# Kernel optimization log

Measured on AMD Instinct MI355X. Metric: run time of the kernel, lower is better.

The kernel has to match this reference:

```python
import jax, jax.numpy as jnp
import numpy as np

FP8_MAX = 448.0   # torch.finfo(float8_e4m3fn).max
BLK = 128         # block_size = [128, 128] for weights; [1, 128] for activations
E, H, I, T, TOPK = 8, 2048, 1408, 512, 2
FP8 = jnp.float8_e4m3fn


def fp8_round(x):
    """Round-trip through float8_e4m3fn (simulates .to(float8_e4m3fn))."""
    return jnp.clip(x, -FP8_MAX, FP8_MAX).astype(FP8).astype(jnp.float32)


def setup_inputs() -> dict:
    key = jax.random.key(0)
    ks = jax.random.split(key, 7)
    hidden_states = jax.random.normal(ks[0], (T, H), jnp.float32)
    top_k_index = jax.random.randint(ks[1], (T, TOPK), 0, E)
    top_k_weights = jax.random.uniform(ks[2], (T, TOPK), jnp.float32)
    # FP8 weight codes (stored as fp32 values exactly representable in e4m3fn)
    gate_up_proj = fp8_round(jax.random.normal(ks[3], (E, 2 * I, H), jnp.float32))
    gate_up_proj_scale_inv = jax.random.uniform(ks[4], (E, (2 * I) // BLK, H // BLK), jnp.float32, 1e-4, 1e-2)
    down_proj = fp8_round(jax.random.normal(ks[5], (E, H, I), jnp.float32))
    down_proj_scale_inv = jax.random.uniform(ks[6], (E, H // BLK, I // BLK), jnp.float32, 1e-4, 1e-2)
    return {
        "hidden_states": hidden_states,
        "top_k_index": top_k_index,
        "top_k_weights": top_k_weights,
        "gate_up_proj": gate_up_proj,
        "gate_up_proj_scale_inv": gate_up_proj_scale_inv,
        "down_proj": down_proj,
        "down_proj_scale_inv": down_proj_scale_inv,
    }


def dequant_weight(wq, s):
    # wq: [E, N, K] fp8 codes; s: [E, N//BLK, K//BLK] per-128x128-block scale_inv
    e, n, k = wq.shape
    wb = wq.reshape(e, n // BLK, BLK, k // BLK, BLK)
    return (wb * s[:, :, None, :, None]).reshape(e, n, k)


def quant_dequant_act(x):
    # dynamic per-(row, 128-block) fp8 activation quantization, then dequant
    shp = x.shape
    xb = x.reshape(shp[:-1] + (shp[-1] // BLK, BLK))
    amax = jnp.max(jnp.abs(xb), axis=-1, keepdims=True)
    scale = jnp.maximum(amax, 1e-12) / FP8_MAX
    q = fp8_round(xb / scale)
    return (q * scale).reshape(shp)


def reference(hidden_states, top_k_index, top_k_weights, gate_up_proj,
              gate_up_proj_scale_inv, down_proj, down_proj_scale_inv):
    w_gu = dequant_weight(gate_up_proj, gate_up_proj_scale_inv)  # [E, 2I, H]
    w_d = dequant_weight(down_proj, down_proj_scale_inv)         # [E, H, I]
    # activation quantization is per-token-block, so unrouted tokens are
    # unaffected; dense per-expert compute + combine-weight mask equals the
    # original gather/scatter loop exactly (unrouted contributions weight 0).
    x = quant_dequant_act(hidden_states)                         # [T, H]
    gate_up = jnp.einsum('th,enh->etn', x, w_gu)                 # [E, T, 2I]
    gate, up = jnp.split(gate_up, 2, axis=-1)
    h = jax.nn.silu(gate) * up                                   # [E, T, I]
    h = quant_dequant_act(h)
    down = jnp.einsum('eti,ehi->eth', h, w_d)                    # [E, T, H]
    # combine[t, e] = sum over top-k slots routing token t to expert e
    combine = jnp.sum(jax.nn.one_hot(top_k_index, E, dtype=top_k_weights.dtype)
                      * top_k_weights[..., None], axis=1)        # [T, E]
    out = jnp.einsum('eth,te->th', down, combine)
    return out.astype(hidden_states.dtype)
```

## Files before the change

### kernel.cpp

```cpp
#include <hip/hip_runtime.h>
#include <math.h>

#define NE 8
#define HD 2048
#define ID 1408
#define NT 512
#define FP8MAX 448.0f

typedef __attribute__((ext_vector_type(4))) float floatx4;

__device__ __forceinline__ floatx4 fzero4() {
    floatx4 z; z.x = 0.f; z.y = 0.f; z.z = 0.f; z.w = 0.f; return z;
}

#define OFF_OFFS  0
#define OFF_TOK   1024
#define OFF_WGT   8192
#define OFF_ENT   16384
#define OFF_XSG   32768
#define OFF_XG    131072
#define OFF_HS    (3*1024*1024)
#define OFF_HQ    (3*1024*1024 + 65536)
#define OFF_GU0   (5*1024*1024)
#define OFF_GU1   (17*1024*1024)

#define LDA 136

__global__ void route_kernel(const int* __restrict__ tki,
                             const float* __restrict__ tkw,
                             int* __restrict__ offs,
                             int* __restrict__ tok,
                             float* __restrict__ wgt,
                             int* __restrict__ ent) {
    __shared__ int cnt[NE];
    __shared__ int cur[NE];
    __shared__ int base[NE + 1];
    int tid = threadIdx.x;
    if (tid < NE) { cnt[tid] = 0; cur[tid] = 0; }
    __syncthreads();
    int e = tki[tid];
    atomicAdd(&cnt[e], 1);
    __syncthreads();
    if (tid == 0) {
        int s = 0;
        for (int i = 0; i < NE; i++) { base[i] = s; s += cnt[i]; }
        base[NE] = s;
    }
    __syncthreads();
    int pos = atomicAdd(&cur[e], 1);
    int j = base[e] + pos;
    tok[j] = tid >> 1;
    wgt[j] = tkw[tid];
    ent[tid] = j;
    if (tid <= NE) offs[tid] = base[tid];
}

__global__ void quant_x_kernel(const float* __restrict__ x,
                               const int* __restrict__ ent,
                               unsigned char* __restrict__ xg,
                               float* __restrict__ xsg) {
    int wid = (blockIdx.x * 256 + threadIdx.x) >> 6;
    int lane = threadIdx.x & 63;
    int t = wid >> 4;
    int b = wid & 15;
    const float2 v = *(const float2*)(x + (long)t * HD + b * 128 + lane * 2);
    float am = fmaxf(fabsf(v.x), fabsf(v.y));
    #pragma unroll
    for (int m = 32; m; m >>= 1) am = fmaxf(am, __shfl_xor(am, m));
    float scale = fmaxf(am, 1e-12f) / FP8MAX;
    int p = __builtin_amdgcn_cvt_pk_fp8_f32(v.x / scale, v.y / scale, 0, false);
    unsigned short pk = (unsigned short)(p & 0xffff);
    int e0 = ent[2 * t], e1 = ent[2 * t + 1];
    *(unsigned short*)(xg + (long)e0 * HD + b * 128 + lane * 2) = pk;
    *(unsigned short*)(xg + (long)e1 * HD + b * 128 + lane * 2) = pk;
    if (lane == 0) { xsg[e0 * 16 + b] = scale; xsg[e1 * 16 + b] = scale; }
}

__global__ void quant_h_kernel(const float* __restrict__ gu0,
                               const float* __restrict__ gu1,
                               unsigned char* __restrict__ hq,
                               float* __restrict__ hs) {
    int wid = (blockIdx.x * 256 + threadIdx.x) >> 6;
    int lane = threadIdx.x & 63;
    int j = wid / 11;
    int b = wid - j * 11;
    long base = (long)j * 2816 + b * 128 + lane * 2;
    float2 ga = *(const float2*)(gu0 + base);
    float2 gb = *(const float2*)(gu1 + base);
    float2 ua = *(const float2*)(gu0 + base + 1408);
    float2 ub = *(const float2*)(gu1 + base + 1408);
    float gx = ga.x + gb.x, gy = ga.y + gb.y;
    float ux = ua.x + ub.x, uy = ua.y + ub.y;
    float hx = (gx / (1.0f + expf(-gx))) * ux;
    float hy = (gy / (1.0f + expf(-gy))) * uy;
    float am = fmaxf(fabsf(hx), fabsf(hy));
    #pragma unroll
    for (int m = 32; m; m >>= 1) am = fmaxf(am, __shfl_xor(am, m));
    float scale = fmaxf(am, 1e-12f) / FP8MAX;
    int p = __builtin_amdgcn_cvt_pk_fp8_f32(hx / scale, hy / scale, 0, false);
    *(unsigned short*)(hq + (long)j * ID + b * 128 + lane * 2) =
        (unsigned short)(p & 0xffff);
    if (lane == 0) hs[j * 11 + b] = scale;
}

__global__ __launch_bounds__(256, 3) void gemm1_kernel(
    const unsigned char* __restrict__ xg,
    const float* __restrict__ xsg,
    const float* __restrict__ wgu,
    const float* __restrict__ sgu,
    const int* __restrict__ offs,
    float* __restrict__ gu0,
    float* __restrict__ gu1) {
    int e = blockIdx.z;
    int mt = blockIdx.y;
    int jb = blockIdx.x >> 1;
    int kh = blockIdx.x & 1;
    int o0 = offs[e], o1 = offs[e + 1];
    int ne = o1 - o0;
    int m0 = mt * 128;
    if (m0 >= ne) return;
    int rem = ne - m0;
    int j0 = o0 + m0;

    __shared__ __align__(16) unsigned char Asm[128 * LDA];
    __shared__ __align__(16) unsigned char Bsm[64 * LDA];
    __shared__ __align__(16) float sxa[128 * 20];

    int tid = threadIdx.x;
    {
        int r = tid >> 1, q = tid & 1;
        int j = j0 + r; if (j >= o1) j = o0;
        float4 s0 = *(const float4*)(xsg + j * 16 + q * 8);
        float4 s1 = *(const float4*)(xsg + j * 16 + q * 8 + 4);
        *(float4*)&sxa[r * 20 + q * 8] = s0;
        *(float4*)&sxa[r * 20 + q * 8 + 4] = s1;
    }

    int wave = tid >> 6;
    int lane = tid & 63;
    int lr = lane & 15;
    int lq = lane >> 4;

    int aseg = tid & 7;
    int arow0 = tid >> 3;
    const unsigned char* aBase0;
    const unsigned char* aBase1;
    const unsigned char* aBase2;
    const unsigned char* aBase3;
    {
        int j;
        j = j0 + arow0;       if (j >= o1) j = o0; aBase0 = xg + (long)j * HD + aseg * 16;
        j = j0 + 32 + arow0;  if (j >= o1) j = o0; aBase1 = xg + (long)j * HD + aseg * 16;
        j = j0 + 64 + arow0;  if (j >= o1) j = o0; aBase2 = xg + (long)j * HD + aseg * 16;
        j = j0 + 96 + arow0;  if (j >= o1) j = o0; aBase3 = xg + (long)j * HD + aseg * 16;
    }

    int bcol = tid & 31;
    int brow0 = tid >> 5;
    const float* bG = wgu + ((long)e * 2816 + jb * 32 + brow0) * HD + bcol * 4;
    const float* bU = wgu + ((long)e * 2816 + 1408 + jb * 32 + brow0) * HD + bcol * 4;
    const float* sgp = sgu + (e * 22 + (jb >> 2)) * 16;
    const float* sup = sgu + (e * 22 + 11 + (jb >> 2)) * 16;

    floatx4 facc[8];
    #pragma unroll
    for (int i = 0; i < 8; i++) facc[i] = fzero4();

    int kbS = kh * 8, kbE = kbS + 8;

    uint4 a0 = *(const uint4*)(aBase0 + kbS * 128);
    uint4 a1 = *(const uint4*)(aBase1 + kbS * 128);
    uint4 a2 = *(const uint4*)(aBase2 + kbS * 128);
    uint4 a3 = *(const uint4*)(aBase3 + kbS * 128);
    float4 f0 = *(const float4*)(bG + kbS * 128);
    float4 f1 = *(const float4*)(bG + kbS * 128 + 8 * HD);
    float4 f2 = *(const float4*)(bG + kbS * 128 + 16 * HD);
    float4 f3 = *(const float4*)(bG + kbS * 128 + 24 * HD);
    float4 f4 = *(const float4*)(bU + kbS * 128);
    float4 f5 = *(const float4*)(bU + kbS * 128 + 8 * HD);
    float4 f6 = *(const float4*)(bU + kbS * 128 + 16 * HD);
    float4 f7 = *(const float4*)(bU + kbS * 128 + 24 * HD);

    for (int kb = kbS; kb < kbE; kb++) {
        {
            *(uint4*)(&Asm[(arow0)      * LDA + aseg * 16]) = a0;
            *(uint4*)(&Asm[(arow0 + 32) * LDA + aseg * 16]) = a1;
            *(uint4*)(&Asm[(arow0 + 64) * LDA + aseg * 16]) = a2;
            *(uint4*)(&Asm[(arow0 + 96) * LDA + aseg * 16]) = a3;
            int p0 = __builtin_amdgcn_cvt_pk_fp8_f32(f0.x, f0.y, 0, false);
            p0 = __builtin_amdgcn_cvt_pk_fp8_f32(f0.z, f0.w, p0, true);
            int p1 = __builtin_amdgcn_cvt_pk_fp8_f32(f1.x, f1.y, 0, false);
            p1 = __builtin_amdgcn_cvt_pk_fp8_f32(f1.z, f1.w, p1, true);
            int p2 = __builtin_amdgcn_cvt_pk_fp8_f32(f2.x, f2.y, 0, false);
            p2 = __builtin_amdgcn_cvt_pk_fp8_f32(f2.z, f2.w, p2, true);
            int p3 = __builtin_amdgcn_cvt_pk_fp8_f32(f3.x, f3.y, 0, false);
            p3 = __builtin_amdgcn_cvt_pk_fp8_f32(f3.z, f3.w, p3, true);
            int p4 = __builtin_amdgcn_cvt_pk_fp8_f32(f4.x, f4.y, 0, false);
            p4 = __builtin_amdgcn_cvt_pk_fp8_f32(f4.z, f4.w, p4, true);
            int p5 = __builtin_amdgcn_cvt_pk_fp8_f32(f5.x, f5.y, 0, false);
            p5 = __builtin_amdgcn_cvt_pk_fp8_f32(f5.z, f5.w, p5, true);
            int p6 = __builtin_amdgcn_cvt_pk_fp8_f32(f6.x, f6.y, 0, false);
            p6 = __builtin_amdgcn_cvt_pk_fp8_f32(f6.z, f6.w, p6, true);
            int p7 = __builtin_amdgcn_cvt_pk_fp8_f32(f7.x, f7.y, 0, false);
            p7 = __builtin_amdgcn_cvt_pk_fp8_f32(f7.z, f7.w, p7, true);
            *(unsigned int*)(&Bsm[(brow0)      * LDA + bcol * 4]) = (unsigned int)p0;
            *(unsigned int*)(&Bsm[(brow0 + 8)  * LDA + bcol * 4]) = (unsigned int)p1;
            *(unsigned int*)(&Bsm[(brow0 + 16) * LDA + bcol * 4]) = (unsigned int)p2;
            *(unsigned int*)(&Bsm[(brow0 + 24) * LDA + bcol * 4]) = (unsigned int)p3;
            *(unsigned int*)(&Bsm[(brow0 + 32) * LDA + bcol * 4]) = (unsigned int)p4;
            *(unsigned int*)(&Bsm[(brow0 + 40) * LDA + bcol * 4]) = (unsigned int)p5;
            *(unsigned int*)(&Bsm[(brow0 + 48) * LDA + bcol * 4]) = (unsigned int)p6;
            *(unsigned int*)(&Bsm[(brow0 + 56) * LDA + bcol * 4]) = (unsigned int)p7;
        }
        __syncthreads();
        {
            int kn = (kb + 1 < kbE) ? (kb + 1) : kb;
            a0 = *(const uint4*)(aBase0 + kn * 128);
            a1 = *(const uint4*)(aBase1 + kn * 128);
            a2 = *(const uint4*)(aBase2 + kn * 128);
            a3 = *(const uint4*)(aBase3 + kn * 128);
            f0 = *(const float4*)(bG + kn * 128);
            f1 = *(const float4*)(bG + kn * 128 + 8 * HD);
            f2 = *(const float4*)(bG + kn * 128 + 16 * HD);
            f3 = *(const float4*)(bG + kn * 128 + 24 * HD);
            f4 = *(const float4*)(bU + kn * 128);
            f5 = *(const float4*)(bU + kn * 128 + 8 * HD);
            f6 = *(const float4*)(bU + kn * 128 + 16 * HD);
            f7 = *(const float4*)(bU + kn * 128 + 24 * HD);
        }
        floatx4 cacc[8];
        #pragma unroll
        for (int i = 0; i < 8; i++) cacc[i] = fzero4();
        #pragma unroll
        for (int ks = 0; ks < 4; ks++) {
            long a[2], b[4];
            #pragma unroll
            for (int mi = 0; mi < 2; mi++)
                a[mi] = *(const long*)(&Asm[(wave * 32 + mi * 16 + lr) * LDA + ks * 32 + lq * 8]);
            #pragma unroll
            for (int ni = 0; ni < 4; ni++)
                b[ni] = *(const long*)(&Bsm[(ni * 16 + lr) * LDA + ks * 32 + lq * 8]);
            #pragma unroll
            for (int mi = 0; mi < 2; mi++)
                #pragma unroll
                for (int ni = 0; ni < 4; ni++)
                    cacc[mi * 4 + ni] = __builtin_amdgcn_mfma_f32_16x16x32_fp8_fp8(
                        a[mi], b[ni], cacc[mi * 4 + ni], 0, 0, 0);
        }
        float sg = sgp[kb];
        float su = sup[kb];
        #pragma unroll
        for (int mi = 0; mi < 2; mi++) {
            #pragma unroll
            for (int reg = 0; reg < 4; reg++) {
                float sx = sxa[(wave * 32 + mi * 16 + lq * 4 + reg) * 20 + kb];
                #pragma unroll
                for (int ni = 0; ni < 4; ni++) {
                    float sw = (ni < 2) ? sg : su;
                    facc[mi * 4 + ni][reg] += cacc[mi * 4 + ni][reg] * (sw * sx);
                }
            }
        }
        __syncthreads();
    }

    float* gu = kh ? gu1 : gu0;
    #pragma unroll
    for (int mi = 0; mi < 2; mi++) {
        #pragma unroll
        for (int ni = 0; ni < 4; ni++) {
            #pragma unroll
            for (int reg = 0; reg < 4; reg++) {
                int r = wave * 32 + mi * 16 + lq * 4 + reg;
                if (r < rem) {
                    long base = (long)(j0 + r) * 2816;
                    long col = (ni < 2) ? (jb * 32 + ni * 16 + lr)
                                        : (1408 + jb * 32 + (ni - 2) * 16 + lr);
                    gu[base + col] = facc[mi * 4 + ni][reg];
                }
            }
        }
    }
}

__global__ __launch_bounds__(256, 4) void gemm2_kernel(
    const unsigned char* __restrict__ hq,
    const float* __restrict__ hs,
    const float* __restrict__ wd,
    const float* __restrict__ sd,
    const int* __restrict__ offs,
    const int* __restrict__ tok,
    const float* __restrict__ wgt,
    float* __restrict__ out) {
    int e = blockIdx.z;
    int mt = blockIdx.y;
    int jb = blockIdx.x >> 1;
    int kh = blockIdx.x & 1;
    int o0 = offs[e], o1 = offs[e + 1];
    int ne = o1 - o0;
    int m0 = mt * 128;
    if (m0 >= ne) return;
    int rem = ne - m0;
    int j0 = o0 + m0;

    __shared__ __align__(16) unsigned char Asm[128 * LDA];
    __shared__ __align__(16) unsigned char Bsm[32 * LDA];
    __shared__ __align__(16) float sha[128 * 12];
    __shared__ int tokL[128];
    __shared__ float wgtL[128];

    int tid = threadIdx.x;
    if (tid < 128) {
        int j = j0 + tid;
        int valid = j < o1;
        if (!valid) j = o0;
        tokL[tid] = tok[j];
        wgtL[tid] = valid ? wgt[j] : 0.0f;
        const float* s = hs + j * 11;
        #pragma unroll
        for (int k = 0; k < 11; k++) sha[tid * 12 + k] = s[k];
    }

    int wave = tid >> 6;
    int lane = tid & 63;
    int lr = lane & 15;
    int lq = lane >> 4;

    int aseg = tid & 7;
    int arow0 = tid >> 3;
    const unsigned char* aBase0;
    const unsigned char* aBase1;
    const unsigned char* aBase2;
    const unsigned char* aBase3;
    {
        int j;
        j = j0 + arow0;       if (j >= o1) j = o0; aBase0 = hq + (long)j * ID + aseg * 16;
        j = j0 + 32 + arow0;  if (j >= o1) j = o0; aBase1 = hq + (long)j * ID + aseg * 16;
        j = j0 + 64 + arow0;  if (j >= o1) j = o0; aBase2 = hq + (long)j * ID + aseg * 16;
        j = j0 + 96 + arow0;  if (j >= o1) j = o0; aBase3 = hq + (long)j * ID + aseg * 16;
    }

    int bcol = tid & 31;
    int brow0 = tid >> 5;
    const float* bB = wd + ((long)e * HD + jb * 32 + brow0) * ID + bcol * 4;
    const float* sdp = sd + (e * 16 + (jb >> 2)) * 11;

    floatx4 facc[4];
    #pragma unroll
    for (int i = 0; i < 4; i++) facc[i] = fzero4();

    int kb0 = kh ? 6 : 0, kb1 = kh ? 11 : 6;

    float4 f0 = *(const float4*)(bB + kb0 * 128);
    float4 f1 = *(const float4*)(bB + kb0 * 128 + 8 * ID);
    float4 f2 = *(const float4*)(bB + kb0 * 128 + 16 * ID);
    float4 f3 = *(const float4*)(bB + kb0 * 128 + 24 * ID);

    for (int kb = kb0; kb < kb1; kb++) {
        {
            uint4 a0 = *(const uint4*)(aBase0 + kb * 128);
            uint4 a1 = *(const uint4*)(aBase1 + kb * 128);
            uint4 a2 = *(const uint4*)(aBase2 + kb * 128);
            uint4 a3 = *(const uint4*)(aBase3 + kb * 128);
            *(uint4*)(&Asm[(arow0)      * LDA + aseg * 16]) = a0;
            *(uint4*)(&Asm[(arow0 + 32) * LDA + aseg * 16]) = a1;
            *(uint4*)(&Asm[(arow0 + 64) * LDA + aseg * 16]) = a2;
            *(uint4*)(&Asm[(arow0 + 96) * LDA + aseg * 16]) = a3;
            int p0 = __builtin_amdgcn_cvt_pk_fp8_f32(f0.x, f0.y, 0, false);
            p0 = __builtin_amdgcn_cvt_pk_fp8_f32(f0.z, f0.w, p0, true);
            int p1 = __builtin_amdgcn_cvt_pk_fp8_f32(f1.x, f1.y, 0, false);
            p1 = __builtin_amdgcn_cvt_pk_fp8_f32(f1.z, f1.w, p1, true);
            int p2 = __builtin_amdgcn_cvt_pk_fp8_f32(f2.x, f2.y, 0, false);
            p2 = __builtin_amdgcn_cvt_pk_fp8_f32(f2.z, f2.w, p2, true);
            int p3 = __builtin_amdgcn_cvt_pk_fp8_f32(f3.x, f3.y, 0, false);
            p3 = __builtin_amdgcn_cvt_pk_fp8_f32(f3.z, f3.w, p3, true);
            *(unsigned int*)(&Bsm[(brow0)      * LDA + bcol * 4]) = (unsigned int)p0;
            *(unsigned int*)(&Bsm[(brow0 + 8)  * LDA + bcol * 4]) = (unsigned int)p1;
            *(unsigned int*)(&Bsm[(brow0 + 16) * LDA + bcol * 4]) = (unsigned int)p2;
            *(unsigned int*)(&Bsm[(brow0 + 24) * LDA + bcol * 4]) = (unsigned int)p3;
        }
        __syncthreads();
        {
            int kn = (kb + 1 < kb1) ? (kb + 1) : kb;
            f0 = *(const float4*)(bB + kn * 128);
            f1 = *(const float4*)(bB + kn * 128 + 8 * ID);
            f2 = *(const float4*)(bB + kn * 128 + 16 * ID);
            f3 = *(const float4*)(bB + kn * 128 + 24 * ID);
        }
        floatx4 cacc[4];
        #pragma unroll
        for (int i = 0; i < 4; i++) cacc[i] = fzero4();
        #pragma unroll
        for (int ks = 0; ks < 4; ks++) {
            long a[2], b[2];
            #pragma unroll
            for (int mi = 0; mi < 2; mi++)
                a[mi] = *(const long*)(&Asm[(wave * 32 + mi * 16 + lr) * LDA + ks * 32 + lq * 8]);
            #pragma unroll
            for (int ni = 0; ni < 2; ni++)
                b[ni] = *(const long*)(&Bsm[(ni * 16 + lr) * LDA + ks * 32 + lq * 8]);
            #pragma unroll
            for (int mi = 0; mi < 2; mi++)
                #pragma unroll
                for (int ni = 0; ni < 2; ni++)
                    cacc[mi * 2 + ni] = __builtin_amdgcn_mfma_f32_16x16x32_fp8_fp8(
                        a[mi], b[ni], cacc[mi * 2 + ni], 0, 0, 0);
        }
        float sw = sdp[kb];
        #pragma unroll
        for (int mi = 0; mi < 2; mi++) {
            #pragma unroll
            for (int reg = 0; reg < 4; reg++) {
                float sh = sha[(wave * 32 + mi * 16 + lq * 4 + reg) * 12 + kb];
                #pragma unroll
                for (int ni = 0; ni < 2; ni++)
                    facc[mi * 2 + ni][reg] += cacc[mi * 2 + ni][reg] * (sw * sh);
            }
        }
        __syncthreads();
    }

    #pragma unroll
    for (int mi = 0; mi < 2; mi++) {
        #pragma unroll
        for (int ni = 0; ni < 2; ni++) {
            #pragma unroll
            for (int reg = 0; reg < 4; reg++) {
                int r = wave * 32 + mi * 16 + lq * 4 + reg;
                if (r < rem) {
                    float v = facc[mi * 2 + ni][reg] * wgtL[r];
                    atomicAdd(out + (long)tokL[r] * HD + jb * 32 + ni * 16 + lr, v);
                }
            }
        }
    }
}

extern "C" void kernel_launch(void* const* d_in, const int* in_sizes, int n_in,
                              void* d_out, int out_size, void* d_ws, size_t ws_size,
                              hipStream_t stream) {
    (void)in_sizes; (void)n_in; (void)out_size; (void)ws_size;
    const float* x   = (const float*)d_in[0];
    const int*   tki = (const int*)d_in[1];
    const float* tkw = (const float*)d_in[2];
    const float* wgu = (const float*)d_in[3];
    const float* sgu = (const float*)d_in[4];
    const float* wd  = (const float*)d_in[5];
    const float* sd  = (const float*)d_in[6];
    float* out = (float*)d_out;
    char* ws = (char*)d_ws;

    int*   offs = (int*)(ws + OFF_OFFS);
    int*   tok  = (int*)(ws + OFF_TOK);
    float* wgt  = (float*)(ws + OFF_WGT);
    int*   ent  = (int*)(ws + OFF_ENT);
    float* xsg  = (float*)(ws + OFF_XSG);
    unsigned char* xg = (unsigned char*)(ws + OFF_XG);
    float* hs   = (float*)(ws + OFF_HS);
    unsigned char* hq = (unsigned char*)(ws + OFF_HQ);
    float* gu0  = (float*)(ws + OFF_GU0);
    float* gu1  = (float*)(ws + OFF_GU1);

    hipMemsetAsync(d_out, 0, (size_t)NT * HD * sizeof(float), stream);
    route_kernel<<<1, 1024, 0, stream>>>(tki, tkw, offs, tok, wgt, ent);
    quant_x_kernel<<<2048, 256, 0, stream>>>(x, ent, xg, xsg);
    gemm1_kernel<<<dim3(88, 8, NE), 256, 0, stream>>>(xg, xsg, wgu, sgu, offs, gu0, gu1);
    quant_h_kernel<<<2816, 256, 0, stream>>>(gu0, gu1, hq, hs);
    gemm2_kernel<<<dim3(128, 8, NE), 256, 0, stream>>>(hq, hs, wd, sd, offs, tok, wgt, out);
}
```

Before: 362.6 us.

## Replace gemm2 atomic scatter with per-slot stores plus combine kernel

gemm2 no longer scales by routing weight and atomically adds into the output. Each K-half now writes plain stores into per-slot buffers that reuse the gate/up workspace. A new combine kernel gathers the two slots per token, sums both K-halves and applies the top-k weights with vectorized loads. The output memset goes away. The aim is to remove atomic contention and the zero-fill, at the cost of an extra kernel launch and about 16 MB of additional global memory traffic.

```diff
diff --git a/kernel.cpp b/kernel.cpp
--- a/kernel.cpp
+++ b/kernel.cpp
@@ -289,9 +289,8 @@
     const float* __restrict__ wd,
     const float* __restrict__ sd,
     const int* __restrict__ offs,
-    const int* __restrict__ tok,
-    const float* __restrict__ wgt,
-    float* __restrict__ out) {
+    float* __restrict__ d0,
+    float* __restrict__ d1) {
     int e = blockIdx.z;
     int mt = blockIdx.y;
     int jb = blockIdx.x >> 1;
@@ -306,16 +305,11 @@
     __shared__ __align__(16) unsigned char Asm[128 * LDA];
     __shared__ __align__(16) unsigned char Bsm[32 * LDA];
     __shared__ __align__(16) float sha[128 * 12];
-    __shared__ int tokL[128];
-    __shared__ float wgtL[128];
 
     int tid = threadIdx.x;
     if (tid < 128) {
         int j = j0 + tid;
-        int valid = j < o1;
-        if (!valid) j = o0;
-        tokL[tid] = tok[j];
-        wgtL[tid] = valid ? wgt[j] : 0.0f;
+        if (j >= o1) j = o0;
         const float* s = hs + j * 11;
         #pragma unroll
         for (int k = 0; k < 11; k++) sha[tid * 12 + k] = s[k];
@@ -420,6 +414,7 @@
         __syncthreads();
     }
 
+    float* dp = kh ? d1 : d0;
     #pragma unroll
     for (int mi = 0; mi < 2; mi++) {
         #pragma unroll
@@ -428,12 +423,36 @@
             for (int reg = 0; reg < 4; reg++) {
                 int r = wave * 32 + mi * 16 + lq * 4 + reg;
                 if (r < rem) {
-                    float v = facc[mi * 2 + ni][reg] * wgtL[r];
-                    atomicAdd(out + (long)tokL[r] * HD + jb * 32 + ni * 16 + lr, v);
+                    dp[(long)(j0 + r) * HD + jb * 32 + ni * 16 + lr] =
+                        facc[mi * 2 + ni][reg];
                 }
             }
         }
     }
+}
+
+__global__ void combine_kernel(const float* __restrict__ d0,
+                               const float* __restrict__ d1,
+                               const int* __restrict__ ent,
+                               const float* __restrict__ tkw,
+                               float* __restrict__ out) {
+    int gid = blockIdx.x * 256 + threadIdx.x;
+    int t = gid >> 9;
+    int c4 = gid & 511;
+    int j0 = ent[2 * t], j1 = ent[2 * t + 1];
+    float w0 = tkw[2 * t], w1 = tkw[2 * t + 1];
+    long b0 = (long)j0 * HD + c4 * 4;
+    long b1 = (long)j1 * HD + c4 * 4;
+    float4 a0 = *(const float4*)(d0 + b0);
+    float4 a1 = *(const float4*)(d1 + b0);
+    float4 a2 = *(const float4*)(d0 + b1);
+    float4 a3 = *(const float4*)(d1 + b1);
+    float4 r;
+    r.x = w0 * (a0.x + a1.x) + w1 * (a2.x + a3.x);
+    r.y = w0 * (a0.y + a1.y) + w1 * (a2.y + a3.y);
+    r.z = w0 * (a0.z + a1.z) + w1 * (a2.z + a3.z);
+    r.w = w0 * (a0.w + a1.w) + w1 * (a2.w + a3.w);
+    *(float4*)(out + (long)t * HD + c4 * 4) = r;
 }
 
 extern "C" void kernel_launch(void* const* d_in, const int* in_sizes, int n_in,
@@ -460,11 +479,13 @@
     unsigned char* hq = (unsigned char*)(ws + OFF_HQ);
     float* gu0  = (float*)(ws + OFF_GU0);
     float* gu1  = (float*)(ws + OFF_GU1);
-
-    hipMemsetAsync(d_out, 0, (size_t)NT * HD * sizeof(float), stream);
+    float* dp0  = (float*)(ws + OFF_GU0);
+    float* dp1  = (float*)(ws + OFF_GU1);
+
     route_kernel<<<1, 1024, 0, stream>>>(tki, tkw, offs, tok, wgt, ent);
     quant_x_kernel<<<2048, 256, 0, stream>>>(x, ent, xg, xsg);
     gemm1_kernel<<<dim3(88, 8, NE), 256, 0, stream>>>(xg, xsg, wgu, sgu, offs, gu0, gu1);
     quant_h_kernel<<<2816, 256, 0, stream>>>(gu0, gu1, hq, hs);
-    gemm2_kernel<<<dim3(128, 8, NE), 256, 0, stream>>>(hq, hs, wd, sd, offs, tok, wgt, out);
-}
+    gemm2_kernel<<<dim3(128, 8, NE), 256, 0, stream>>>(hq, hs, wd, sd, offs, dp0, dp1);
+    combine_kernel<<<1024, 256, 0, stream>>>(dp0, dp1, ent, tkw, out);
+}
```

New measurement: 362.3 us. No clear change (-0.1%).
